# Performance work log

Hardware: AMD Instinct MI355X
Metric: run time of the kernel (lower is better)

Reference implementation:

```python
import jax, jax.numpy as jnp
import numpy as np
from jax import lax

C = 128
KS = 9
PAD = KS // 2


def _conv1d(r, w):
    # r: [B, C, L], w: [Cout, Cin, K] -> [B, C, L], SAME padding
    return lax.conv_general_dilated(r, w, window_strides=(1,), padding=[(PAD, PAD)],
                                    dimension_numbers=("NCH", "OIH", "NCH"))


def _pass_once(x, w, vertical, reverse):
    # x: [B, C, H, W]; scan sequentially along H (vertical) or W (horizontal).
    if not vertical:
        x = jnp.transpose(x, (0, 1, 3, 2))  # scan axis -> axis 2
    if reverse:
        x = jnp.flip(x, axis=2)
    xs = jnp.moveaxis(x, 2, 0)  # [S, B, C, L]

    def step(carry, xi):
        y = xi + jax.nn.relu(_conv1d(carry, w))
        return y, y

    _, ys = lax.scan(step, xs[0], xs[1:])
    out = jnp.concatenate([xs[:1], ys], axis=0)
    out = jnp.moveaxis(out, 0, 2)
    if reverse:
        out = jnp.flip(out, axis=2)
    if not vertical:
        out = jnp.transpose(out, (0, 1, 3, 2))
    return out


def setup_inputs() -> dict:
    key = jax.random.key(0)
    kx, k1, k2, k3, k4 = jax.random.split(key, 5)
    B, H, W = 8, 128, 256
    std = (1.0 / (C * KS)) ** 0.5  # kaiming_normal_(a=1) scale
    x = jax.random.normal(kx, (B, C, H, W), dtype=jnp.float32)
    w_ud = jax.random.normal(k1, (C, C, KS), dtype=jnp.float32) * std
    w_du = jax.random.normal(k2, (C, C, KS), dtype=jnp.float32) * std
    w_lr = jax.random.normal(k3, (C, C, KS), dtype=jnp.float32) * std
    w_rl = jax.random.normal(k4, (C, C, KS), dtype=jnp.float32) * std
    return {"x": x, "w_ud": w_ud, "w_du": w_du, "w_lr": w_lr, "w_rl": w_rl}


def reference(x, w_ud, w_du, w_lr, w_rl):
    # Order matches torch ModuleList: up_down, down_up, left_right, right_left
    x = _pass_once(x, w_ud, vertical=True, reverse=False)
    x = _pass_once(x, w_du, vertical=True, reverse=True)
    x = _pass_once(x, w_lr, vertical=False, reverse=False)
    x = _pass_once(x, w_rl, vertical=False, reverse=True)
    return x
```

## Files before the change

kernel.cpp:

```cpp
#include <hip/hip_runtime.h>

#define C_ 128
#define KS_ 9
#define B_ 8
#define H_ 128
#define W_ 256
#define HW_ (H_ * W_)
#define CHW_ (C_ * HW_)

typedef _Float16 half8 __attribute__((ext_vector_type(8)));
typedef float floatx4 __attribute__((ext_vector_type(4)));
typedef unsigned long long ull;

#define F16_IMG_BYTES 67108864u

#define WS_WF_OFF    0u
#define WS_WF_BYTES  1179648u
#define WS_CARRY_OFF 1183744u
#define CARRY_HALVES (8 * 256 * 128)
#define WS_YT_OFF    2232320u
#define WS_NEED      (WS_YT_OFF + F16_IMG_BYTES)

__device__ __forceinline__ int imin(int a, int b) { return a < b ? a : b; }
__device__ __forceinline__ int imax(int a, int b) { return a > b ? a : b; }

__global__ void k_copy(const float* __restrict__ in, float* __restrict__ out, int n4) {
  int i = blockIdx.x * blockDim.x + threadIdx.x;
  int stride = gridDim.x * blockDim.x;
  const floatx4* ip = (const floatx4*)in;
  floatx4* op = (floatx4*)out;
  for (; i < n4; i += stride) op[i] = ip[i];
}

__global__ void k_wprep(const float* w0, const float* w1, const float* w2, const float* w3,
                        _Float16* __restrict__ wf) {
  const float* Wp[4] = {w0, w1, w2, w3};
  const float* W = Wp[blockIdx.y];
  _Float16* out = wf + (size_t)blockIdx.y * (8 * 36 * 64 * 8);
  int idx = blockIdx.x * 256 + threadIdx.x;
  if (idx >= 8 * 36 * 64 * 8) return;
  int j = idx & 7;
  int lane = (idx >> 3) & 63;
  int ks = (idx >> 9) % 36;
  int mt = (idx >> 9) / 36;
  int co = mt * 16 + (lane & 15);
  int k = ks * 32 + ((lane >> 4) & 3) * 8 + j;
  int kk = k >> 7, ci = k & 127;
  out[idx] = (_Float16)W[((size_t)co * C_ + ci) * KS_ + kk];
}

template <typename XT, typename YT>
__global__ void k_carry0(const XT* __restrict__ imgX, YT* __restrict__ imgY,
                         _Float16* __restrict__ cout_, int S, int L, int istart) {
  int b = blockIdx.y;
  int e = blockIdx.x * 256 + threadIdx.x;
  if (e >= L * 16) return;
  int col = e >> 4, ci0 = (e & 15) * 8;
  union { ull u[2]; _Float16 h[8]; } pk;
#pragma unroll
  for (int u2 = 0; u2 < 8; ++u2) {
    size_t off = ((size_t)(b * C_ + ci0 + u2) * S + istart) * L + col;
    float v = (float)imgX[off];
    pk.h[u2] = (_Float16)v;
    imgY[off] = (YT)v;
  }
  ull* dst = (ull*)(cout_ + ((size_t)b * L + col) * 128 + ci0);
  dst[0] = pk.u[0];
  dst[1] = pk.u[1];
}

__global__ void k_t1h(const _Float16* __restrict__ in, _Float16* __restrict__ out) {
  __shared__ _Float16 tile[32][33];
  size_t pbase = (size_t)blockIdx.z * HW_;
  int h0 = blockIdx.y * 32, w0 = blockIdx.x * 32;
  int tx = threadIdx.x, ty = threadIdx.y;
  for (int i = 0; i < 32; i += 8)
    tile[ty + i][tx] = in[pbase + (size_t)(h0 + ty + i) * W_ + (w0 + tx)];
  __syncthreads();
  for (int i = 0; i < 32; i += 8)
    out[pbase + (size_t)(w0 + ty + i) * H_ + (h0 + tx)] = tile[tx][ty + i];
}

__global__ void k_t2(const _Float16* __restrict__ in, float* __restrict__ out) {
  __shared__ float tile[32][33];
  size_t pbase = (size_t)blockIdx.z * HW_;
  int h0 = blockIdx.y * 32, w0 = blockIdx.x * 32;
  int tx = threadIdx.x, ty = threadIdx.y;
  for (int i = 0; i < 32; i += 8)
    tile[ty + i][tx] = (float)in[pbase + (size_t)(w0 + ty + i) * H_ + (h0 + tx)];
  __syncthreads();
  for (int i = 0; i < 32; i += 8)
    out[pbase + (size_t)(h0 + ty + i) * W_ + (w0 + tx)] = tile[tx][ty + i];
}

template <typename XT, typename YT, int WC, int MAXT>
__global__ __launch_bounds__(512, 2) void k_scan3(
    const XT* __restrict__ imgX, YT* __restrict__ imgY,
    const _Float16* __restrict__ Wf, const _Float16* __restrict__ cin,
    _Float16* __restrict__ cout_,
    int S, int L, int n0, int nsteps, int dir, int istart) {
  constexpr int MAXW = WC + 72;
  constexpr int BSZ = MAXW * 132;
  __shared__ _Float16 Bl[2][BSZ];
  const int c0 = blockIdx.x * WC;
  const int b = blockIdx.y;
  const int t = threadIdx.x;
  const int lane = t & 63, wave = t >> 6;
  const int q = lane >> 4, m = lane & 15;

  half8 A_[36];
  {
    const half8* wp2 = (const half8*)Wf;
#pragma unroll
    for (int ks = 0; ks < 36; ++ks)
      A_[ks] = wp2[(wave * 36 + ks) * 64 + lane];
  }

  for (int i = t * 8; i < BSZ; i += 4096) {
    ull* z0 = (ull*)(&Bl[0][i]);
    ull* z1 = (ull*)(&Bl[1][i]);
    z0[0] = 0ull; z0[1] = 0ull;
    z1[0] = 0ull; z1[1] = 0ull;
  }
  __syncthreads();

  {
    const int NCH = (WC + 64) * 16;
    for (int e = t; e < NCH; e += 512) {
      const int lcol = e >> 4;
      const int col = c0 - 32 + lcol;
      if (col >= 0 && col < L) {
        const int ci0 = (e & 15) * 8;
        const ull* src = (const ull*)(cin + ((size_t)b * L + col) * 128 + ci0);
        ull* dst = (ull*)(&Bl[0][(lcol + 4) * 132 + ci0]);
        dst[0] = src[0];
        dst[1] = src[1];
      }
    }
  }
  __syncthreads();

  int cur = 0;
  for (int p = 1; p <= nsteps; ++p) {
    const int row = istart + dir * (n0 + p);
    const int ext = 32 - 4 * p;
    const int lo = imax(c0 - ext, 0);
    const int hi = imin(c0 + WC + ext, L);
    const int tt0 = -((c0 - lo + 15) >> 4);
    const int ntile = ((hi - c0 + 15) >> 4) - tt0;
    const _Float16* BR = Bl[cur];
    _Float16* BW = Bl[cur ^ 1];
    const size_t rbase = ((size_t)(b * C_ + wave * 16) * S + row) * L;

    float xv[MAXT][4];
#pragma unroll
    for (int u = 0; u < MAXT; ++u) {
      if (u >= ntile) break;
      const int col = c0 + (tt0 + u) * 16 + m;
      const bool ld2 = (col >= lo) && (col < hi);
#pragma unroll
      for (int r = 0; r < 4; ++r)
        xv[u][r] = ld2 ? (float)imgX[rbase + (size_t)(q * 4 + r) * (S * L) + col] : 0.f;
    }

#pragma unroll
    for (int u = 0; u < MAXT; ++u) {
      if (u >= ntile) break;
      const int ti = tt0 + u;
      floatx4 aA = {0.f, 0.f, 0.f, 0.f}, aB = {0.f, 0.f, 0.f, 0.f};
      const int lbase = ti * 16 + m + 32;
#pragma unroll
      for (int ks2 = 0; ks2 < 18; ++ks2) {
        const int ksA = 2 * ks2, ksB = 2 * ks2 + 1;
        {
          const int kk = ksA >> 2, ci0 = (ksA & 3) * 32 + q * 8;
          const ull* bp = (const ull*)(BR + (lbase + kk) * 132 + ci0);
          union { ull u2[2]; half8 v; } bf;
          bf.u2[0] = bp[0]; bf.u2[1] = bp[1];
          aA = __builtin_amdgcn_mfma_f32_16x16x32_f16(A_[ksA], bf.v, aA, 0, 0, 0);
        }
        {
          const int kk = ksB >> 2, ci0 = (ksB & 3) * 32 + q * 8;
          const ull* bp = (const ull*)(BR + (lbase + kk) * 132 + ci0);
          union { ull u2[2]; half8 v; } bf;
          bf.u2[0] = bp[0]; bf.u2[1] = bp[1];
          aB = __builtin_amdgcn_mfma_f32_16x16x32_f16(A_[ksB], bf.v, aB, 0, 0, 0);
        }
      }
      const int col = c0 + ti * 16 + m;
      const bool instrip = (col >= c0) && (col < c0 + WC);
      const bool inlds = (col >= lo) && (col < hi);
      union { ull uu; _Float16 h[4]; } pk;
#pragma unroll
      for (int r = 0; r < 4; ++r) {
        const float y = xv[u][r] + fmaxf(aA[r] + aB[r], 0.f);
        pk.h[r] = (_Float16)y;
        if (instrip)
          imgY[rbase + (size_t)(q * 4 + r) * (S * L) + col] = (YT)y;
      }
      if (inlds)
        *(ull*)(BW + (col - c0 + 36) * 132 + wave * 16 + q * 4) = pk.uu;
    }
    __syncthreads();
    cur ^= 1;
  }

  {
    const _Float16* BP = Bl[cur];
    for (int e = t; e < WC * 16; e += 512) {
      const int lc = e >> 4, ci0 = (e & 15) * 8;
      ull* dst = (ull*)(cout_ + ((size_t)b * L + (c0 + lc)) * 128 + ci0);
      const ull* src = (const ull*)(BP + (lc + 36) * 132 + ci0);
      dst[0] = src[0];
      dst[1] = src[1];
    }
  }
}

__device__ __forceinline__ void gemm_acc_fb(const _Float16* Bl, const _Float16* __restrict__ Wfrag,
                                            int wrow_base, int lane, floatx4* acc) {
  const int q = lane >> 4;
  const half8* wfp = (const half8*)Wfrag + lane;
  for (int ks = 0; ks < 36; ++ks) {
    int k0 = ks * 32 + q * 8;
    int kk = k0 >> 7;
    int ci0 = k0 & 127;
    half8 bf = *(const half8*)&Bl[(size_t)(wrow_base + kk) * C_ + ci0];
    const half8* wp = wfp + ks * 64;
#pragma unroll
    for (int mt = 0; mt < 8; ++mt)
      acc[mt] = __builtin_amdgcn_mfma_f32_16x16x32_f16(wp[mt * 36 * 64], bf, acc[mt], 0, 0, 0);
  }
}

__global__ __launch_bounds__(256) void k_step_v(float* __restrict__ Y,
                                                const _Float16* __restrict__ Wfrag,
                                                int row, int prev) {
  __shared__ _Float16 Bl[80 * 128];
  const int b = blockIdx.y, w0 = blockIdx.x * 64, t = threadIdx.x;
  {
    const float* base = Y + (size_t)b * CHW_ + (size_t)prev * W_;
#pragma unroll
    for (int it = 0; it < 10; ++it) {
      int c = it * 256 + t;
      int ci = c / 20, c4 = c % 20;
      int wst = w0 - 8 + c4 * 4;
      const float* p = base + (size_t)ci * HW_ + wst;
      float v[4];
      if (wst >= 0 && wst + 4 <= W_) {
        floatx4 u = *(const floatx4*)p;
        v[0] = u[0]; v[1] = u[1]; v[2] = u[2]; v[3] = u[3];
      } else {
#pragma unroll
        for (int j = 0; j < 4; ++j) { int w = wst + j; v[j] = (w >= 0 && w < W_) ? p[j] : 0.f; }
      }
      int wl = c4 * 4;
#pragma unroll
      for (int j = 0; j < 4; ++j) Bl[(wl + j) * C_ + ci] = (_Float16)v[j];
    }
  }
  __syncthreads();
  const int lane = t & 63, wave = t >> 6, q = lane >> 4, l15 = lane & 15;
  floatx4 acc[8];
#pragma unroll
  for (int mt = 0; mt < 8; ++mt) acc[mt] = (floatx4){0.f, 0.f, 0.f, 0.f};
  gemm_acc_fb(Bl, Wfrag, wave * 16 + l15 + 4, lane, acc);
  const int wcol = w0 + wave * 16 + l15;
#pragma unroll
  for (int mt = 0; mt < 8; ++mt)
#pragma unroll
    for (int r = 0; r < 4; ++r) {
      int co = mt * 16 + q * 4 + r;
      size_t off = (size_t)b * CHW_ + (size_t)co * HW_ + (size_t)row * W_ + wcol;
      Y[off] = Y[off] + fmaxf(acc[mt][r], 0.f);
    }
}

__global__ __launch_bounds__(256) void k_step_h(float* __restrict__ Y,
                                                const _Float16* __restrict__ Wfrag,
                                                int row, int prev) {
  __shared__ _Float16 Bl[80 * 128];
  const int b = blockIdx.y, h0 = blockIdx.x * 64, t = threadIdx.x;
  {
    const float* base = Y + (size_t)b * CHW_ + prev;
    for (int e = t; e < 80 * 128; e += 256) {
      int hl = e >> 7, ci = e & 127, h = h0 - 8 + hl;
      float v = 0.f;
      if (h >= 0 && h < H_) v = base[(size_t)ci * HW_ + (size_t)h * W_];
      Bl[hl * C_ + ci] = (_Float16)v;
    }
  }
  __syncthreads();
  const int lane = t & 63, wave = t >> 6, q = lane >> 4, l15 = lane & 15;
  floatx4 acc[8];
#pragma unroll
  for (int mt = 0; mt < 8; ++mt) acc[mt] = (floatx4){0.f, 0.f, 0.f, 0.f};
  gemm_acc_fb(Bl, Wfrag, wave * 16 + l15 + 4, lane, acc);
  const int hc = h0 + wave * 16 + l15;
#pragma unroll
  for (int mt = 0; mt < 8; ++mt)
#pragma unroll
    for (int r = 0; r < 4; ++r) {
      int co = mt * 16 + q * 4 + r;
      size_t off = (size_t)b * CHW_ + (size_t)co * HW_ + (size_t)hc * W_ + row;
      Y[off] = Y[off] + fmaxf(acc[mt][r], 0.f);
    }
}

extern "C" void kernel_launch(void* const* d_in, const int* in_sizes, int n_in,
                              void* d_out, int out_size, void* d_ws, size_t ws_size,
                              hipStream_t stream) {
  const float* x = (const float*)d_in[0];
  const float* w_ud = (const float*)d_in[1];
  const float* w_du = (const float*)d_in[2];
  const float* w_lr = (const float*)d_in[3];
  const float* w_rl = (const float*)d_in[4];

  float* Y = (float*)d_out;
  char* ws = (char*)d_ws;
  _Float16* Wf = (_Float16*)(ws + WS_WF_OFF);
  _Float16* carryA = (_Float16*)(ws + WS_CARRY_OFF);
  _Float16* carryB = carryA + CARRY_HALVES;
  _Float16* YtA = (_Float16*)(ws + WS_YT_OFF);
  _Float16* F16A = (_Float16*)d_out;
  _Float16* F16B = (_Float16*)((char*)d_out + F16_IMG_BYTES);

  const size_t WF_PASS = 8 * 36 * 64 * 8;

  k_wprep<<<dim3(576, 4), 256, 0, stream>>>(w_ud, w_du, w_lr, w_rl, Wf);

  if (ws_size >= WS_NEED) {
    _Float16* cb_[2] = {carryA, carryB};
    k_carry0<float, float><<<dim3(16, B_), 256, 0, stream>>>(x, Y, carryA, H_, W_, 0);
    for (int n0 = 0, j = 0; n0 < H_ - 1; n0 += 8, ++j) {
      int ns = H_ - 1 - n0; if (ns > 8) ns = 8;
      k_scan3<float, float, 16, 5><<<dim3(16, B_), 512, 0, stream>>>(
          x, Y, Wf + 0 * WF_PASS, cb_[j & 1], cb_[(j + 1) & 1], H_, W_, n0, ns, +1, 0);
    }
    k_carry0<float, _Float16><<<dim3(16, B_), 256, 0, stream>>>(Y, YtA, carryA, H_, W_, H_ - 1);
    for (int n0 = 0, j = 0; n0 < H_ - 1; n0 += 8, ++j) {
      int ns = H_ - 1 - n0; if (ns > 8) ns = 8;
      k_scan3<float, _Float16, 16, 5><<<dim3(16, B_), 512, 0, stream>>>(
          Y, YtA, Wf + 1 * WF_PASS, cb_[j & 1], cb_[(j + 1) & 1], H_, W_, n0, ns, -1, H_ - 1);
    }
    k_t1h<<<dim3(8, 4, B_ * C_), dim3(32, 8), 0, stream>>>(YtA, F16A);
    k_carry0<_Float16, _Float16><<<dim3(8, B_), 256, 0, stream>>>(F16A, YtA, carryA, W_, H_, 0);
    for (int n0 = 0, j = 0; n0 < W_ - 1; n0 += 8, ++j) {
      int ns = W_ - 1 - n0; if (ns > 8) ns = 8;
      k_scan3<_Float16, _Float16, 8, 5><<<dim3(16, B_), 512, 0, stream>>>(
          F16A, YtA, Wf + 2 * WF_PASS, cb_[j & 1], cb_[(j + 1) & 1], W_, H_, n0, ns, +1, 0);
    }
    k_carry0<_Float16, _Float16><<<dim3(8, B_), 256, 0, stream>>>(YtA, F16B, carryA, W_, H_, W_ - 1);
    for (int n0 = 0, j = 0; n0 < W_ - 1; n0 += 8, ++j) {
      int ns = W_ - 1 - n0; if (ns > 8) ns = 8;
      k_scan3<_Float16, _Float16, 8, 5><<<dim3(16, B_), 512, 0, stream>>>(
          YtA, F16B, Wf + 3 * WF_PASS, cb_[j & 1], cb_[(j + 1) & 1], W_, H_, n0, ns, -1, W_ - 1);
    }
    k_copy<<<2048, 256, 0, stream>>>((const float*)F16B, (float*)YtA, F16_IMG_BYTES / 16);
    k_t2<<<dim3(8, 4, B_ * C_), dim3(32, 8), 0, stream>>>(YtA, Y);
  } else {
    k_copy<<<2048, 256, 0, stream>>>(x, Y, B_ * C_ * H_ * W_ / 4);
    for (int i = 1; i < H_; ++i)
      k_step_v<<<dim3(W_ / 64, B_), 256, 0, stream>>>(Y, Wf + 0 * WF_PASS, i, i - 1);
    for (int i = H_ - 2; i >= 0; --i)
      k_step_v<<<dim3(W_ / 64, B_), 256, 0, stream>>>(Y, Wf + 1 * WF_PASS, i, i + 1);
    for (int i = 1; i < W_; ++i)
      k_step_h<<<dim3(H_ / 64, B_), 256, 0, stream>>>(Y, Wf + 2 * WF_PASS, i, i - 1);
    for (int i = W_ - 2; i >= 0; --i)
      k_step_h<<<dim3(H_ / 64, B_), 256, 0, stream>>>(Y, Wf + 3 * WF_PASS, i, i + 1);
  }
}
```

Baseline: 4.923 ms.

## Split scan K-reduction across wave pairs and halve strip width to double blocks

Each wave now computes two output-channel groups over half of the reduction (18 of 36 k-steps), then exchanges partial sums with its partner wave through LDS and a block barrier. The strip width per block is halved and the grid doubled (32 blocks per batch), so more CUs work on the sequential scan. The cost is an extra __syncthreads per column tile and more halo recomputation per block, since each narrower strip still carries the 32-column halo on each side.

```diff
diff --git a/kernel.cpp b/kernel.cpp
--- a/kernel.cpp
+++ b/kernel.cpp
@@ -102,18 +102,23 @@
   constexpr int MAXW = WC + 72;
   constexpr int BSZ = MAXW * 132;
   __shared__ _Float16 Bl[2][BSZ];
+  __shared__ floatx4 Sc[2][8][64];
   const int c0 = blockIdx.x * WC;
   const int b = blockIdx.y;
   const int t = threadIdx.x;
   const int lane = t & 63, wave = t >> 6;
   const int q = lane >> 4, m = lane & 15;
-
-  half8 A_[36];
+  const int h = wave & 1;
+  const int g = wave >> 1;
+
+  half8 A0[18], A1[18];
   {
     const half8* wp2 = (const half8*)Wf;
 #pragma unroll
-    for (int ks = 0; ks < 36; ++ks)
-      A_[ks] = wp2[(wave * 36 + ks) * 64 + lane];
+    for (int i = 0; i < 18; ++i) {
+      A0[i] = wp2[((g * 2 + 0) * 36 + h * 18 + i) * 64 + lane];
+      A1[i] = wp2[((g * 2 + 1) * 36 + h * 18 + i) * 64 + lane];
+    }
   }
 
   for (int i = t * 8; i < BSZ; i += 4096) {
@@ -170,31 +175,27 @@
       floatx4 aA = {0.f, 0.f, 0.f, 0.f}, aB = {0.f, 0.f, 0.f, 0.f};
       const int lbase = ti * 16 + m + 32;
 #pragma unroll
-      for (int ks2 = 0; ks2 < 18; ++ks2) {
-        const int ksA = 2 * ks2, ksB = 2 * ks2 + 1;
-        {
-          const int kk = ksA >> 2, ci0 = (ksA & 3) * 32 + q * 8;
-          const ull* bp = (const ull*)(BR + (lbase + kk) * 132 + ci0);
-          union { ull u2[2]; half8 v; } bf;
-          bf.u2[0] = bp[0]; bf.u2[1] = bp[1];
-          aA = __builtin_amdgcn_mfma_f32_16x16x32_f16(A_[ksA], bf.v, aA, 0, 0, 0);
-        }
-        {
-          const int kk = ksB >> 2, ci0 = (ksB & 3) * 32 + q * 8;
-          const ull* bp = (const ull*)(BR + (lbase + kk) * 132 + ci0);
-          union { ull u2[2]; half8 v; } bf;
-          bf.u2[0] = bp[0]; bf.u2[1] = bp[1];
-          aB = __builtin_amdgcn_mfma_f32_16x16x32_f16(A_[ksB], bf.v, aB, 0, 0, 0);
-        }
+      for (int i = 0; i < 18; ++i) {
+        const int ks = h * 18 + i;
+        const int kk = ks >> 2;
+        const int ci0 = (ks & 3) * 32 + q * 8;
+        const ull* bp = (const ull*)(BR + (lbase + kk) * 132 + ci0);
+        union { ull u2[2]; half8 v; } bf;
+        bf.u2[0] = bp[0]; bf.u2[1] = bp[1];
+        aA = __builtin_amdgcn_mfma_f32_16x16x32_f16(A0[i], bf.v, aA, 0, 0, 0);
+        aB = __builtin_amdgcn_mfma_f32_16x16x32_f16(A1[i], bf.v, aB, 0, 0, 0);
       }
+      Sc[u & 1][wave][lane] = h ? aA : aB;
+      __syncthreads();
+      const floatx4 ac = (h ? aB : aA) + Sc[u & 1][wave ^ 1][lane];
       const int col = c0 + ti * 16 + m;
       const bool instrip = (col >= c0) && (col < c0 + WC);
       const bool inlds = (col >= lo) && (col < hi);
-      union { ull uu; _Float16 h[4]; } pk;
+      union { ull uu; _Float16 h4[4]; } pk;
 #pragma unroll
       for (int r = 0; r < 4; ++r) {
-        const float y = xv[u][r] + fmaxf(aA[r] + aB[r], 0.f);
-        pk.h[r] = (_Float16)y;
+        const float y = xv[u][r] + fmaxf(ac[r], 0.f);
+        pk.h4[r] = (_Float16)y;
         if (instrip)
           imgY[rbase + (size_t)(q * 4 + r) * (S * L) + col] = (YT)y;
       }
@@ -334,26 +335,26 @@
     k_carry0<float, float><<<dim3(16, B_), 256, 0, stream>>>(x, Y, carryA, H_, W_, 0);
     for (int n0 = 0, j = 0; n0 < H_ - 1; n0 += 8, ++j) {
       int ns = H_ - 1 - n0; if (ns > 8) ns = 8;
-      k_scan3<float, float, 16, 5><<<dim3(16, B_), 512, 0, stream>>>(
+      k_scan3<float, float, 8, 5><<<dim3(32, B_), 512, 0, stream>>>(
           x, Y, Wf + 0 * WF_PASS, cb_[j & 1], cb_[(j + 1) & 1], H_, W_, n0, ns, +1, 0);
     }
     k_carry0<float, _Float16><<<dim3(16, B_), 256, 0, stream>>>(Y, YtA, carryA, H_, W_, H_ - 1);
     for (int n0 = 0, j = 0; n0 < H_ - 1; n0 += 8, ++j) {
       int ns = H_ - 1 - n0; if (ns > 8) ns = 8;
-      k_scan3<float, _Float16, 16, 5><<<dim3(16, B_), 512, 0, stream>>>(
+      k_scan3<float, _Float16, 8, 5><<<dim3(32, B_), 512, 0, stream>>>(
           Y, YtA, Wf + 1 * WF_PASS, cb_[j & 1], cb_[(j + 1) & 1], H_, W_, n0, ns, -1, H_ - 1);
     }
     k_t1h<<<dim3(8, 4, B_ * C_), dim3(32, 8), 0, stream>>>(YtA, F16A);
     k_carry0<_Float16, _Float16><<<dim3(8, B_), 256, 0, stream>>>(F16A, YtA, carryA, W_, H_, 0);
     for (int n0 = 0, j = 0; n0 < W_ - 1; n0 += 8, ++j) {
       int ns = W_ - 1 - n0; if (ns > 8) ns = 8;
-      k_scan3<_Float16, _Float16, 8, 5><<<dim3(16, B_), 512, 0, stream>>>(
+      k_scan3<_Float16, _Float16, 4, 5><<<dim3(32, B_), 512, 0, stream>>>(
           F16A, YtA, Wf + 2 * WF_PASS, cb_[j & 1], cb_[(j + 1) & 1], W_, H_, n0, ns, +1, 0);
     }
     k_carry0<_Float16, _Float16><<<dim3(8, B_), 256, 0, stream>>>(YtA, F16B, carryA, W_, H_, W_ - 1);
     for (int n0 = 0, j = 0; n0 < W_ - 1; n0 += 8, ++j) {
       int ns = W_ - 1 - n0; if (ns > 8) ns = 8;
-      k_scan3<_Float16, _Float16, 8, 5><<<dim3(16, B_), 512, 0, stream>>>(
+      k_scan3<_Float16, _Float16, 4, 5><<<dim3(32, B_), 512, 0, stream>>>(
           YtA, F16B, Wf + 3 * WF_PASS, cb_[j & 1], cb_[(j + 1) & 1], W_, H_, n0, ns, -1, W_ - 1);
     }
     k_copy<<<2048, 256, 0, stream>>>((const float*)F16B, (float*)YtA, F16_IMG_BYTES / 16);
```

New measurement: 4.215 ms. -14.4%, faster.
